# Kernel tuning notes

Measured on AMD Instinct MI355X. Metric: run time of the kernel, lower is better.

Reference implementation:

```python
import jax, jax.numpy as jnp
import numpy as np

D = 2048        # hidden_size
F = 1024        # moe_intermediate_size
E = 16          # num_experts
TOP_K = 2       # num_experts_per_tok
NORM_TOPK = True
B, S = 2, 1024


def setup_inputs() -> dict:
    key = jax.random.key(0)
    ks = jax.random.split(key, 6)
    scale = 0.02
    x = jax.random.normal(ks[0], (B, S, D), jnp.float32)
    w_gate = jax.random.normal(ks[1], (D, E), jnp.float32) * scale          # gate Linear (no bias)
    w_g = jax.random.normal(ks[2], (E, D, F), jnp.float32) * scale          # SwitchGLU gate_proj
    w_u = jax.random.normal(ks[3], (E, D, F), jnp.float32) * scale          # SwitchGLU up_proj
    w_d = jax.random.normal(ks[4], (E, F, D), jnp.float32) * scale          # SwitchGLU down_proj
    expert_bias = jnp.zeros((E,), jnp.float32)                              # nn.Parameter(zeros)
    return {"x": x, "w_gate": w_gate, "w_g": w_g, "w_u": w_u, "w_d": w_d,
            "expert_bias": expert_bias}


def reference(x, w_gate, w_g, w_u, w_d, expert_bias):
    xf = x.reshape(-1, D)  # [T, D] flatten tokens
    T = xf.shape[0]
    # routing: softmax in fp32, bias added AFTER softmax (as in source)
    gates = jax.nn.softmax((xf @ w_gate).astype(jnp.float32), axis=-1) + expert_bias
    scores, inds = jax.lax.top_k(gates, TOP_K)  # values gathered from biased gates
    if NORM_TOPK:
        scores = scores / (jnp.sum(scores, axis=-1, keepdims=True) + 1e-20)
    scores = scores.astype(x.dtype)
    # scatter top-k weights into dense [T, E] combine matrix (top-k inds are distinct)
    cw = jnp.zeros((T, E), x.dtype).at[jnp.arange(T)[:, None], inds].add(scores)
    # scan over experts: each step one gated-SiLU MLP + weighted accumulate
    def step(acc, inp):
        wg, wu, wd, w = inp  # wg/wu [D,F], wd [F,D], w [T]
        h = jax.nn.silu(xf @ wg) * (xf @ wu)  # [T, F]
        return acc + w[:, None] * (h @ wd), None
    y, _ = jax.lax.scan(step, jnp.zeros_like(xf), (w_g, w_u, w_d, cw.T))
    return y.reshape(x.shape)
```

## Files before the change

### kernel.cpp

```cpp
#include <hip/hip_runtime.h>
#include <hip/hip_bf16.h>

#define D_DIM 2048
#define F_DIM 1024
#define E_NUM 16
#define T_TOK 2048

typedef float f32x4 __attribute__((ext_vector_type(4)));
typedef short short8 __attribute__((ext_vector_type(8)));

__device__ inline unsigned pk2bf(float a, float b) {
    __hip_bfloat162 h2 = __float22bfloat162_rn(make_float2(a, b));
    union { __hip_bfloat162 h; unsigned u; } c; c.h = h2; return c.u;
}

__global__ __launch_bounds__(64) void k_route(const float* __restrict__ x,
                                              const float* __restrict__ wg,
                                              const float* __restrict__ bias,
                                              int* __restrict__ topk_idx,
                                              float* __restrict__ topk_w,
                                              int* __restrict__ counts) {
    int t = blockIdx.x;
    int l = threadIdx.x;
    int e = l & 15, c = l >> 4;
    const float* xr = x + (size_t)t * D_DIM + c * (D_DIM / 4);
    const float* wr = wg + (size_t)(c * (D_DIM / 4)) * E_NUM + e;
    float acc = 0.f;
#pragma unroll 4
    for (int d = 0; d < D_DIM / 4; ++d) acc += xr[d] * wr[(size_t)d * E_NUM];
    acc += __shfl_xor(acc, 16);
    acc += __shfl_xor(acc, 32);
    float m = acc;
#pragma unroll
    for (int s = 1; s < 16; s <<= 1) m = fmaxf(m, __shfl_xor(m, s));
    float p = __expf(acc - m);
    float sum = p;
#pragma unroll
    for (int s = 1; s < 16; s <<= 1) sum += __shfl_xor(sum, s);
    p = p / sum + bias[e];
    float v1 = p; int i1 = e;
#pragma unroll
    for (int s = 1; s < 16; s <<= 1) {
        float ov = __shfl_xor(v1, s); int oi = __shfl_xor(i1, s);
        if (ov > v1 || (ov == v1 && oi < i1)) { v1 = ov; i1 = oi; }
    }
    float v2 = (e == i1) ? -1e30f : p; int i2 = e;
#pragma unroll
    for (int s = 1; s < 16; s <<= 1) {
        float ov = __shfl_xor(v2, s); int oi = __shfl_xor(i2, s);
        if (ov > v2 || (ov == v2 && oi < i2)) { v2 = ov; i2 = oi; }
    }
    if (l == 0) {
        float s2 = v1 + v2 + 1e-20f;
        topk_idx[2 * t] = i1; topk_idx[2 * t + 1] = i2;
        topk_w[2 * t] = v1 / s2; topk_w[2 * t + 1] = v2 / s2;
        atomicAdd(&counts[i1], 1);
        atomicAdd(&counts[i2], 1);
    }
}

__global__ void k_offsets(const int* __restrict__ counts, int* __restrict__ offsets,
                          int* __restrict__ cursors) {
    if (threadIdx.x == 0) {
        int run = 0;
        for (int e = 0; e < E_NUM; ++e) { offsets[e] = run; cursors[e] = run; run += counts[e]; }
        offsets[E_NUM] = run;
    }
}

__global__ void k_scatter(const int* __restrict__ topk_idx, const float* __restrict__ topk_w,
                          int* __restrict__ cursors, int* __restrict__ token_ids,
                          float* __restrict__ slot_w) {
    int i = blockIdx.x * blockDim.x + threadIdx.x;
    if (i >= T_TOK * 2) return;
    int e = topk_idx[i];
    int slot = atomicAdd(&cursors[e], 1);
    token_ids[slot] = i >> 1;
    slot_w[slot] = topk_w[i];
}

__global__ __launch_bounds__(256, 4) void k_gateup(const float* __restrict__ x,
                                                   const float* __restrict__ wg_all,
                                                   const float* __restrict__ wu_all,
                                                   const int* __restrict__ offsets,
                                                   const int* __restrict__ token_ids,
                                                   __hip_bfloat16* __restrict__ hbuf) {
    int e = blockIdx.z;
    int off = offsets[e];
    int n_e = offsets[e + 1] - off;
    int m0 = blockIdx.y * 64;
    if (m0 >= n_e) return;
    int n0 = blockIdx.x * 64;
    const float* wg = wg_all + (size_t)e * (D_DIM * F_DIM);
    const float* wu = wu_all + (size_t)e * (D_DIM * F_DIM);

    __shared__ unsigned short As[2][64 * 40];
    __shared__ unsigned short Bs[2][2][64 * 40];

    int tid = threadIdx.x;
    int wid = tid >> 6, lane = tid & 63;
    int q = lane >> 4, nl = lane & 15;
    int wr = wid >> 1, wc = wid & 1;

    int arow = tid >> 2, acg = (tid & 3) * 8;
    int ag = m0 + arow;
    bool avalid = ag < n_e;
    const float* xrow = x + (size_t)token_ids[off + (avalid ? ag : 0)] * D_DIM;
    int bkr = (tid >> 4) * 2;
    int bcol = (tid & 15) * 4;

    f32x4 ra[2], rg[2], ru[2];
    f32x4 accG[2][2], accU[2][2];
#pragma unroll
    for (int ms = 0; ms < 2; ++ms)
#pragma unroll
        for (int ns = 0; ns < 2; ++ns) {
            accG[ms][ns] = (f32x4){0.f, 0.f, 0.f, 0.f};
            accU[ms][ns] = (f32x4){0.f, 0.f, 0.f, 0.f};
        }

    auto loadG = [&](int k0) {
        ra[0] = avalid ? *(const f32x4*)(xrow + k0 + acg) : (f32x4){0.f, 0.f, 0.f, 0.f};
        ra[1] = avalid ? *(const f32x4*)(xrow + k0 + acg + 4) : (f32x4){0.f, 0.f, 0.f, 0.f};
        size_t o0 = (size_t)(k0 + bkr) * F_DIM + n0 + bcol;
        rg[0] = *(const f32x4*)(wg + o0);
        rg[1] = *(const f32x4*)(wg + o0 + F_DIM);
        ru[0] = *(const f32x4*)(wu + o0);
        ru[1] = *(const f32x4*)(wu + o0 + F_DIM);
    };
    auto writeL = [&](int b) {
        union { short8 v; unsigned u[4]; } w0;
        w0.u[0] = pk2bf(ra[0].x, ra[0].y); w0.u[1] = pk2bf(ra[0].z, ra[0].w);
        w0.u[2] = pk2bf(ra[1].x, ra[1].y); w0.u[3] = pk2bf(ra[1].z, ra[1].w);
        *(short8*)&As[b][arow * 40 + acg] = w0.v;
#pragma unroll
        for (int j = 0; j < 4; ++j) {
            int col = bcol + j;
            int kk = bkr ^ (((col >> 3) & 3) << 3);
            *(unsigned*)&Bs[b][0][col * 40 + kk] = pk2bf(rg[0][j], rg[1][j]);
            *(unsigned*)&Bs[b][1][col * 40 + kk] = pk2bf(ru[0][j], ru[1][j]);
        }
    };
    auto compute = [&](int b) {
        short8 af[2];
#pragma unroll
        for (int ms = 0; ms < 2; ++ms)
            af[ms] = *(const short8*)&As[b][(wr * 32 + ms * 16 + nl) * 40 + q * 8];
#pragma unroll
        for (int ns = 0; ns < 2; ++ns) {
            int col = wc * 32 + ns * 16 + nl;
            int colb = col * 40 + 8 * (q ^ ((col >> 3) & 3));
            short8 bg = *(const short8*)&Bs[b][0][colb];
            short8 bu = *(const short8*)&Bs[b][1][colb];
#pragma unroll
            for (int ms = 0; ms < 2; ++ms) {
                accG[ms][ns] = __builtin_amdgcn_mfma_f32_16x16x32_bf16(af[ms], bg, accG[ms][ns], 0, 0, 0);
                accU[ms][ns] = __builtin_amdgcn_mfma_f32_16x16x32_bf16(af[ms], bu, accU[ms][ns], 0, 0, 0);
            }
        }
    };

    loadG(0);
    writeL(0);
    __syncthreads();
    for (int t = 0; t < D_DIM / 32; ++t) {
        int b = t & 1;
        if (t < D_DIM / 32 - 1) loadG((t + 1) * 32);
        compute(b);
        if (t < D_DIM / 32 - 1) writeL(b ^ 1);
        __syncthreads();
    }

#pragma unroll
    for (int ms = 0; ms < 2; ++ms)
#pragma unroll
        for (int j = 0; j < 4; ++j) {
            int g2 = m0 + wr * 32 + ms * 16 + q * 4 + j;
            if (g2 < n_e) {
                size_t hbase = (size_t)(off + g2) * F_DIM;
#pragma unroll
                for (int ns = 0; ns < 2; ++ns) {
                    float g = accG[ms][ns][j];
                    float u = accU[ms][ns][j];
                    float hv = (g / (1.f + __expf(-g))) * u;
                    hbuf[hbase + n0 + wc * 32 + ns * 16 + nl] = __float2bfloat16(hv);
                }
            }
        }
}

__global__ __launch_bounds__(256, 4) void k_down(const __hip_bfloat16* __restrict__ hbuf,
                                                 const float* __restrict__ wd_all,
                                                 const int* __restrict__ offsets,
                                                 const int* __restrict__ token_ids,
                                                 const float* __restrict__ slot_w,
                                                 float* __restrict__ y) {
    int e = blockIdx.z;
    int off = offsets[e];
    int n_e = offsets[e + 1] - off;
    int m0 = blockIdx.y * 64;
    if (m0 >= n_e) return;
    int n0 = blockIdx.x * 64;
    const float* wd = wd_all + (size_t)e * (F_DIM * D_DIM);

    __shared__ unsigned short As[2][64 * 40];
    __shared__ unsigned short Bs[2][64 * 40];

    int tid = threadIdx.x;
    int wid = tid >> 6, lane = tid & 63;
    int q = lane >> 4, nl = lane & 15;
    int wr = wid >> 1, wc = wid & 1;

    int arow = tid >> 2, acg = (tid & 3) * 8;
    int ag = m0 + arow;
    bool avalid = ag < n_e;
    const unsigned short* hrow = (const unsigned short*)hbuf + (size_t)(off + (avalid ? ag : 0)) * F_DIM;
    int bkr = (tid >> 4) * 2;
    int bcol = (tid & 15) * 4;

    short8 rh;
    f32x4 rd[2];
    f32x4 acc[2][2];
#pragma unroll
    for (int ms = 0; ms < 2; ++ms)
#pragma unroll
        for (int ns = 0; ns < 2; ++ns) acc[ms][ns] = (f32x4){0.f, 0.f, 0.f, 0.f};

    auto loadG = [&](int k0) {
        rh = avalid ? *(const short8*)(hrow + k0 + acg) : (short8){0, 0, 0, 0, 0, 0, 0, 0};
        size_t o0 = (size_t)(k0 + bkr) * D_DIM + n0 + bcol;
        rd[0] = *(const f32x4*)(wd + o0);
        rd[1] = *(const f32x4*)(wd + o0 + D_DIM);
    };
    auto writeL = [&](int b) {
        *(short8*)&As[b][arow * 40 + acg] = rh;
#pragma unroll
        for (int j = 0; j < 4; ++j) {
            int col = bcol + j;
            int kk = bkr ^ (((col >> 3) & 3) << 3);
            *(unsigned*)&Bs[b][col * 40 + kk] = pk2bf(rd[0][j], rd[1][j]);
        }
    };
    auto compute = [&](int b) {
        short8 af[2];
#pragma unroll
        for (int ms = 0; ms < 2; ++ms)
            af[ms] = *(const short8*)&As[b][(wr * 32 + ms * 16 + nl) * 40 + q * 8];
#pragma unroll
        for (int ns = 0; ns < 2; ++ns) {
            int col = wc * 32 + ns * 16 + nl;
            short8 bd = *(const short8*)&Bs[b][col * 40 + 8 * (q ^ ((col >> 3) & 3))];
#pragma unroll
            for (int ms = 0; ms < 2; ++ms)
                acc[ms][ns] = __builtin_amdgcn_mfma_f32_16x16x32_bf16(af[ms], bd, acc[ms][ns], 0, 0, 0);
        }
    };

    loadG(0);
    writeL(0);
    __syncthreads();
    for (int t = 0; t < F_DIM / 32; ++t) {
        int b = t & 1;
        if (t < F_DIM / 32 - 1) loadG((t + 1) * 32);
        compute(b);
        if (t < F_DIM / 32 - 1) writeL(b ^ 1);
        __syncthreads();
    }

#pragma unroll
    for (int ms = 0; ms < 2; ++ms)
#pragma unroll
        for (int j = 0; j < 4; ++j) {
            int g2 = m0 + wr * 32 + ms * 16 + q * 4 + j;
            if (g2 < n_e) {
                float w2 = slot_w[off + g2];
                int t = token_ids[off + g2];
#pragma unroll
                for (int ns = 0; ns < 2; ++ns)
                    atomicAdd(&y[(size_t)t * D_DIM + n0 + wc * 32 + ns * 16 + nl], acc[ms][ns][j] * w2);
            }
        }
}

extern "C" void kernel_launch(void* const* d_in, const int* in_sizes, int n_in,
                              void* d_out, int out_size, void* d_ws, size_t ws_size,
                              hipStream_t stream) {
    const float* x      = (const float*)d_in[0];
    const float* w_gate = (const float*)d_in[1];
    const float* w_g    = (const float*)d_in[2];
    const float* w_u    = (const float*)d_in[3];
    const float* w_d    = (const float*)d_in[4];
    const float* bias   = (const float*)d_in[5];
    float* y = (float*)d_out;

    char* ws = (char*)d_ws;
    int*   counts    = (int*)(ws + 0);
    int*   offsets   = (int*)(ws + 64);
    int*   cursors   = (int*)(ws + 192);
    int*   topk_idx  = (int*)(ws + 256);
    float* topk_w    = (float*)(ws + 256 + 16384);
    int*   token_ids = (int*)(ws + 256 + 32768);
    float* slot_w    = (float*)(ws + 256 + 49152);
    __hip_bfloat16* hbuf = (__hip_bfloat16*)(ws + 66048);

    hipMemsetAsync(ws, 0, 256, stream);
    hipMemsetAsync(d_out, 0, (size_t)out_size * sizeof(float), stream);

    k_route<<<T_TOK, 64, 0, stream>>>(x, w_gate, bias, topk_idx, topk_w, counts);
    k_offsets<<<1, 64, 0, stream>>>(counts, offsets, cursors);
    k_scatter<<<(T_TOK * 2 + 255) / 256, 256, 0, stream>>>(topk_idx, topk_w, cursors, token_ids, slot_w);
    k_gateup<<<dim3(F_DIM / 64, 32, E_NUM), 256, 0, stream>>>(x, w_g, w_u, offsets, token_ids, hbuf);
    k_down<<<dim3(D_DIM / 64, 32, E_NUM), 256, 0, stream>>>(hbuf, w_d, offsets, token_ids, slot_w, y);
}
```

Measured before the change: 372.4 us.

## Give each wave a private LDS weight tile and load activations straight to registers

Both expert GEMM kernels drop the block-shared, double-buffered LDS tiles and the per-iteration __syncthreads. Each wavefront now stages its own 32-column slice of the weight tile in a private LDS buffer and reads its activation rows (x or hbuf) directly from global memory into MFMA operand registers. This is meant to remove block-wide barrier stalls and A-tile LDS traffic. In exchange, weight tiles are fetched and converted twice per block and activations are re-read by two waves each. The activation loads are also not prefetched, so their latency sits right before the MFMAs. Launch bounds are lowered from 4 to 3 blocks per CU.

```diff
diff --git a/kernel.cpp b/kernel.cpp
--- a/kernel.cpp
+++ b/kernel.cpp
@@ -8,6 +8,7 @@
 
 typedef float f32x4 __attribute__((ext_vector_type(4)));
 typedef short short8 __attribute__((ext_vector_type(8)));
+typedef unsigned uint2v __attribute__((ext_vector_type(2)));
 
 __device__ inline unsigned pk2bf(float a, float b) {
     __hip_bfloat162 h2 = __float22bfloat162_rn(make_float2(a, b));
@@ -79,7 +80,7 @@
     slot_w[slot] = topk_w[i];
 }
 
-__global__ __launch_bounds__(256, 4) void k_gateup(const float* __restrict__ x,
+__global__ __launch_bounds__(256, 3) void k_gateup(const float* __restrict__ x,
                                                    const float* __restrict__ wg_all,
                                                    const float* __restrict__ wu_all,
                                                    const int* __restrict__ offsets,
@@ -94,22 +95,26 @@
     const float* wg = wg_all + (size_t)e * (D_DIM * F_DIM);
     const float* wu = wu_all + (size_t)e * (D_DIM * F_DIM);
 
-    __shared__ unsigned short As[2][64 * 40];
-    __shared__ unsigned short Bs[2][2][64 * 40];
+    __shared__ unsigned short Bs[4][2][32 * 40];
 
     int tid = threadIdx.x;
     int wid = tid >> 6, lane = tid & 63;
     int q = lane >> 4, nl = lane & 15;
     int wr = wid >> 1, wc = wid & 1;
-
-    int arow = tid >> 2, acg = (tid & 3) * 8;
-    int ag = m0 + arow;
-    bool avalid = ag < n_e;
-    const float* xrow = x + (size_t)token_ids[off + (avalid ? ag : 0)] * D_DIM;
-    int bkr = (tid >> 4) * 2;
-    int bcol = (tid & 15) * 4;
-
-    f32x4 ra[2], rg[2], ru[2];
+    int colbase = n0 + wc * 32;
+
+    int r0 = m0 + wr * 32 + nl;
+    int r1 = r0 + 16;
+    const float* xr0 = x + (size_t)token_ids[off + (r0 < n_e ? r0 : 0)] * D_DIM;
+    const float* xr1 = x + (size_t)token_ids[off + (r1 < n_e ? r1 : 0)] * D_DIM;
+
+    int cg = lane & 7;
+    int kb4 = (lane >> 3) * 4;
+    const float* pg0 = wg + (size_t)kb4 * F_DIM + colbase + cg * 4;
+    const float* pu0 = wu + (size_t)kb4 * F_DIM + colbase + cg * 4;
+    unsigned short* BG = &Bs[wid][0][0];
+    unsigned short* BU = &Bs[wid][1][0];
+
     f32x4 accG[2][2], accU[2][2];
 #pragma unroll
     for (int ms = 0; ms < 2; ++ms)
@@ -119,77 +124,77 @@
             accU[ms][ns] = (f32x4){0.f, 0.f, 0.f, 0.f};
         }
 
-    auto loadG = [&](int k0) {
-        ra[0] = avalid ? *(const f32x4*)(xrow + k0 + acg) : (f32x4){0.f, 0.f, 0.f, 0.f};
-        ra[1] = avalid ? *(const f32x4*)(xrow + k0 + acg + 4) : (f32x4){0.f, 0.f, 0.f, 0.f};
-        size_t o0 = (size_t)(k0 + bkr) * F_DIM + n0 + bcol;
-        rg[0] = *(const f32x4*)(wg + o0);
-        rg[1] = *(const f32x4*)(wg + o0 + F_DIM);
-        ru[0] = *(const f32x4*)(wu + o0);
-        ru[1] = *(const f32x4*)(wu + o0 + F_DIM);
-    };
-    auto writeL = [&](int b) {
-        union { short8 v; unsigned u[4]; } w0;
-        w0.u[0] = pk2bf(ra[0].x, ra[0].y); w0.u[1] = pk2bf(ra[0].z, ra[0].w);
-        w0.u[2] = pk2bf(ra[1].x, ra[1].y); w0.u[3] = pk2bf(ra[1].z, ra[1].w);
-        *(short8*)&As[b][arow * 40 + acg] = w0.v;
+    f32x4 g0, g1, g2, g3, u0, u1, u2, u3;
+    auto loadW = [&](int k0) {
+        const float* pg = pg0 + (size_t)k0 * F_DIM;
+        const float* pu = pu0 + (size_t)k0 * F_DIM;
+        g0 = *(const f32x4*)pg; g1 = *(const f32x4*)(pg + F_DIM);
+        g2 = *(const f32x4*)(pg + 2 * F_DIM); g3 = *(const f32x4*)(pg + 3 * F_DIM);
+        u0 = *(const f32x4*)pu; u1 = *(const f32x4*)(pu + F_DIM);
+        u2 = *(const f32x4*)(pu + 2 * F_DIM); u3 = *(const f32x4*)(pu + 3 * F_DIM);
+    };
+    auto writeW = [&]() {
 #pragma unroll
         for (int j = 0; j < 4; ++j) {
-            int col = bcol + j;
-            int kk = bkr ^ (((col >> 3) & 3) << 3);
-            *(unsigned*)&Bs[b][0][col * 40 + kk] = pk2bf(rg[0][j], rg[1][j]);
-            *(unsigned*)&Bs[b][1][col * 40 + kk] = pk2bf(ru[0][j], ru[1][j]);
-        }
-    };
-    auto compute = [&](int b) {
-        short8 af[2];
-#pragma unroll
-        for (int ms = 0; ms < 2; ++ms)
-            af[ms] = *(const short8*)&As[b][(wr * 32 + ms * 16 + nl) * 40 + q * 8];
+            int col = cg * 4 + j;
+            int kk = kb4 ^ (((col >> 3) & 3) << 3);
+            uint2v vg, vu;
+            vg[0] = pk2bf(g0[j], g1[j]); vg[1] = pk2bf(g2[j], g3[j]);
+            vu[0] = pk2bf(u0[j], u1[j]); vu[1] = pk2bf(u2[j], u3[j]);
+            *(uint2v*)&BG[col * 40 + kk] = vg;
+            *(uint2v*)&BU[col * 40 + kk] = vu;
+        }
+    };
+    auto compute = [&](int k0) {
+        f32x4 a00 = *(const f32x4*)(xr0 + k0 + q * 8);
+        f32x4 a01 = *(const f32x4*)(xr0 + k0 + q * 8 + 4);
+        f32x4 a10 = *(const f32x4*)(xr1 + k0 + q * 8);
+        f32x4 a11 = *(const f32x4*)(xr1 + k0 + q * 8 + 4);
+        union { short8 v; unsigned u[4]; } af0, af1;
+        af0.u[0] = pk2bf(a00.x, a00.y); af0.u[1] = pk2bf(a00.z, a00.w);
+        af0.u[2] = pk2bf(a01.x, a01.y); af0.u[3] = pk2bf(a01.z, a01.w);
+        af1.u[0] = pk2bf(a10.x, a10.y); af1.u[1] = pk2bf(a10.z, a10.w);
+        af1.u[2] = pk2bf(a11.x, a11.y); af1.u[3] = pk2bf(a11.z, a11.w);
 #pragma unroll
         for (int ns = 0; ns < 2; ++ns) {
-            int col = wc * 32 + ns * 16 + nl;
-            int colb = col * 40 + 8 * (q ^ ((col >> 3) & 3));
-            short8 bg = *(const short8*)&Bs[b][0][colb];
-            short8 bu = *(const short8*)&Bs[b][1][colb];
-#pragma unroll
-            for (int ms = 0; ms < 2; ++ms) {
-                accG[ms][ns] = __builtin_amdgcn_mfma_f32_16x16x32_bf16(af[ms], bg, accG[ms][ns], 0, 0, 0);
-                accU[ms][ns] = __builtin_amdgcn_mfma_f32_16x16x32_bf16(af[ms], bu, accU[ms][ns], 0, 0, 0);
-            }
-        }
-    };
-
-    loadG(0);
-    writeL(0);
-    __syncthreads();
+            int col = ns * 16 + nl;
+            int cb = col * 40 + 8 * (q ^ ((col >> 3) & 3));
+            short8 bg = *(const short8*)&BG[cb];
+            short8 bu = *(const short8*)&BU[cb];
+            accG[0][ns] = __builtin_amdgcn_mfma_f32_16x16x32_bf16(af0.v, bg, accG[0][ns], 0, 0, 0);
+            accG[1][ns] = __builtin_amdgcn_mfma_f32_16x16x32_bf16(af1.v, bg, accG[1][ns], 0, 0, 0);
+            accU[0][ns] = __builtin_amdgcn_mfma_f32_16x16x32_bf16(af0.v, bu, accU[0][ns], 0, 0, 0);
+            accU[1][ns] = __builtin_amdgcn_mfma_f32_16x16x32_bf16(af1.v, bu, accU[1][ns], 0, 0, 0);
+        }
+    };
+
+    loadW(0);
+    writeW();
     for (int t = 0; t < D_DIM / 32; ++t) {
-        int b = t & 1;
-        if (t < D_DIM / 32 - 1) loadG((t + 1) * 32);
-        compute(b);
-        if (t < D_DIM / 32 - 1) writeL(b ^ 1);
-        __syncthreads();
+        if (t < D_DIM / 32 - 1) loadW((t + 1) * 32);
+        compute(t * 32);
+        if (t < D_DIM / 32 - 1) writeW();
     }
 
 #pragma unroll
     for (int ms = 0; ms < 2; ++ms)
 #pragma unroll
         for (int j = 0; j < 4; ++j) {
-            int g2 = m0 + wr * 32 + ms * 16 + q * 4 + j;
-            if (g2 < n_e) {
-                size_t hbase = (size_t)(off + g2) * F_DIM;
+            int g2r = m0 + wr * 32 + ms * 16 + q * 4 + j;
+            if (g2r < n_e) {
+                size_t hbase = (size_t)(off + g2r) * F_DIM;
 #pragma unroll
                 for (int ns = 0; ns < 2; ++ns) {
                     float g = accG[ms][ns][j];
                     float u = accU[ms][ns][j];
                     float hv = (g / (1.f + __expf(-g))) * u;
-                    hbuf[hbase + n0 + wc * 32 + ns * 16 + nl] = __float2bfloat16(hv);
+                    hbuf[hbase + colbase + ns * 16 + nl] = __float2bfloat16(hv);
                 }
             }
         }
 }
 
-__global__ __launch_bounds__(256, 4) void k_down(const __hip_bfloat16* __restrict__ hbuf,
+__global__ __launch_bounds__(256, 3) void k_down(const __hip_bfloat16* __restrict__ hbuf,
                                                  const float* __restrict__ wd_all,
                                                  const int* __restrict__ offsets,
                                                  const int* __restrict__ token_ids,
@@ -203,81 +208,77 @@
     int n0 = blockIdx.x * 64;
     const float* wd = wd_all + (size_t)e * (F_DIM * D_DIM);
 
-    __shared__ unsigned short As[2][64 * 40];
-    __shared__ unsigned short Bs[2][64 * 40];
+    __shared__ unsigned short Bs[4][32 * 40];
 
     int tid = threadIdx.x;
     int wid = tid >> 6, lane = tid & 63;
     int q = lane >> 4, nl = lane & 15;
     int wr = wid >> 1, wc = wid & 1;
-
-    int arow = tid >> 2, acg = (tid & 3) * 8;
-    int ag = m0 + arow;
-    bool avalid = ag < n_e;
-    const unsigned short* hrow = (const unsigned short*)hbuf + (size_t)(off + (avalid ? ag : 0)) * F_DIM;
-    int bkr = (tid >> 4) * 2;
-    int bcol = (tid & 15) * 4;
-
-    short8 rh;
-    f32x4 rd[2];
+    int colbase = n0 + wc * 32;
+
+    int r0 = m0 + wr * 32 + nl;
+    int r1 = r0 + 16;
+    const unsigned short* h0 = (const unsigned short*)hbuf + (size_t)(off + (r0 < n_e ? r0 : 0)) * F_DIM;
+    const unsigned short* h1 = (const unsigned short*)hbuf + (size_t)(off + (r1 < n_e ? r1 : 0)) * F_DIM;
+
+    int cg = lane & 7;
+    int kb4 = (lane >> 3) * 4;
+    const float* pd0 = wd + (size_t)kb4 * D_DIM + colbase + cg * 4;
+    unsigned short* BD = &Bs[wid][0];
+
     f32x4 acc[2][2];
 #pragma unroll
     for (int ms = 0; ms < 2; ++ms)
 #pragma unroll
         for (int ns = 0; ns < 2; ++ns) acc[ms][ns] = (f32x4){0.f, 0.f, 0.f, 0.f};
 
-    auto loadG = [&](int k0) {
-        rh = avalid ? *(const short8*)(hrow + k0 + acg) : (short8){0, 0, 0, 0, 0, 0, 0, 0};
-        size_t o0 = (size_t)(k0 + bkr) * D_DIM + n0 + bcol;
-        rd[0] = *(const f32x4*)(wd + o0);
-        rd[1] = *(const f32x4*)(wd + o0 + D_DIM);
-    };
-    auto writeL = [&](int b) {
-        *(short8*)&As[b][arow * 40 + acg] = rh;
+    f32x4 d0, d1, d2, d3;
+    auto loadW = [&](int k0) {
+        const float* pd = pd0 + (size_t)k0 * D_DIM;
+        d0 = *(const f32x4*)pd; d1 = *(const f32x4*)(pd + D_DIM);
+        d2 = *(const f32x4*)(pd + 2 * D_DIM); d3 = *(const f32x4*)(pd + 3 * D_DIM);
+    };
+    auto writeW = [&]() {
 #pragma unroll
         for (int j = 0; j < 4; ++j) {
-            int col = bcol + j;
-            int kk = bkr ^ (((col >> 3) & 3) << 3);
-            *(unsigned*)&Bs[b][col * 40 + kk] = pk2bf(rd[0][j], rd[1][j]);
-        }
-    };
-    auto compute = [&](int b) {
-        short8 af[2];
-#pragma unroll
-        for (int ms = 0; ms < 2; ++ms)
-            af[ms] = *(const short8*)&As[b][(wr * 32 + ms * 16 + nl) * 40 + q * 8];
+            int col = cg * 4 + j;
+            int kk = kb4 ^ (((col >> 3) & 3) << 3);
+            uint2v vd;
+            vd[0] = pk2bf(d0[j], d1[j]); vd[1] = pk2bf(d2[j], d3[j]);
+            *(uint2v*)&BD[col * 40 + kk] = vd;
+        }
+    };
+    auto compute = [&](int k0) {
+        short8 af0 = *(const short8*)(h0 + k0 + q * 8);
+        short8 af1 = *(const short8*)(h1 + k0 + q * 8);
 #pragma unroll
         for (int ns = 0; ns < 2; ++ns) {
-            int col = wc * 32 + ns * 16 + nl;
-            short8 bd = *(const short8*)&Bs[b][col * 40 + 8 * (q ^ ((col >> 3) & 3))];
-#pragma unroll
-            for (int ms = 0; ms < 2; ++ms)
-                acc[ms][ns] = __builtin_amdgcn_mfma_f32_16x16x32_bf16(af[ms], bd, acc[ms][ns], 0, 0, 0);
-        }
-    };
-
-    loadG(0);
-    writeL(0);
-    __syncthreads();
+            int col = ns * 16 + nl;
+            short8 bd = *(const short8*)&BD[col * 40 + 8 * (q ^ ((col >> 3) & 3))];
+            acc[0][ns] = __builtin_amdgcn_mfma_f32_16x16x32_bf16(af0, bd, acc[0][ns], 0, 0, 0);
+            acc[1][ns] = __builtin_amdgcn_mfma_f32_16x16x32_bf16(af1, bd, acc[1][ns], 0, 0, 0);
+        }
+    };
+
+    loadW(0);
+    writeW();
     for (int t = 0; t < F_DIM / 32; ++t) {
-        int b = t & 1;
-        if (t < F_DIM / 32 - 1) loadG((t + 1) * 32);
-        compute(b);
-        if (t < F_DIM / 32 - 1) writeL(b ^ 1);
-        __syncthreads();
+        if (t < F_DIM / 32 - 1) loadW((t + 1) * 32);
+        compute(t * 32);
+        if (t < F_DIM / 32 - 1) writeW();
     }
 
 #pragma unroll
     for (int ms = 0; ms < 2; ++ms)
 #pragma unroll
         for (int j = 0; j < 4; ++j) {
-            int g2 = m0 + wr * 32 + ms * 16 + q * 4 + j;
-            if (g2 < n_e) {
-                float w2 = slot_w[off + g2];
-                int t = token_ids[off + g2];
+            int g2r = m0 + wr * 32 + ms * 16 + q * 4 + j;
+            if (g2r < n_e) {
+                float w2 = slot_w[off + g2r];
+                int t = token_ids[off + g2r];
 #pragma unroll
                 for (int ns = 0; ns < 2; ++ns)
-                    atomicAdd(&y[(size_t)t * D_DIM + n0 + wc * 32 + ns * 16 + nl], acc[ms][ns][j] * w2);
+                    atomicAdd(&y[(size_t)t * D_DIM + colbase + ns * 16 + nl], acc[ms][ns][j] * w2);
             }
         }
 }
```

New measurement: 558.7 us. +50.0%, slower.

## Pre-gather tokens to bf16 buffer and remap block order across XCDs

Applied to the files above, without the earlier changes.

Adds a gather kernel that copies each routed token's row into a contiguous bf16 buffer, so the gate/up GEMM reads packed bf16 rows directly and no longer does the per-row token_ids indirection or the fp32-to-bf16 conversion on the A operand. Both GEMMs now use a flattened 1D grid, and the block index is remapped with a stride of 8 so that blocks sharing the same expert and weight columns are likely placed on the same XCD and its L2. Out-of-range rows are clamped to the last valid slot instead of being zero-filled, so they read real data whose results must be masked out at the output. This costs one extra kernel launch and an 8MB bf16 intermediate.

```diff
diff --git a/kernel.cpp b/kernel.cpp
--- a/kernel.cpp
+++ b/kernel.cpp
@@ -5,6 +5,7 @@
 #define F_DIM 1024
 #define E_NUM 16
 #define T_TOK 2048
+#define NSLOT (T_TOK * 2)
 
 typedef float f32x4 __attribute__((ext_vector_type(4)));
 typedef short short8 __attribute__((ext_vector_type(8)));
@@ -72,25 +73,41 @@
                           int* __restrict__ cursors, int* __restrict__ token_ids,
                           float* __restrict__ slot_w) {
     int i = blockIdx.x * blockDim.x + threadIdx.x;
-    if (i >= T_TOK * 2) return;
+    if (i >= NSLOT) return;
     int e = topk_idx[i];
     int slot = atomicAdd(&cursors[e], 1);
     token_ids[slot] = i >> 1;
     slot_w[slot] = topk_w[i];
 }
 
-__global__ __launch_bounds__(256, 4) void k_gateup(const float* __restrict__ x,
+__global__ __launch_bounds__(256) void k_gather(const float* __restrict__ x,
+                                                const int* __restrict__ token_ids,
+                                                __hip_bfloat16* __restrict__ xg) {
+    int s = blockIdx.x;
+    const float* src = x + (size_t)token_ids[s] * D_DIM + threadIdx.x * 8;
+    f32x4 a = *(const f32x4*)src;
+    f32x4 b = *(const f32x4*)(src + 4);
+    union { short8 v; unsigned u[4]; } w;
+    w.u[0] = pk2bf(a.x, a.y); w.u[1] = pk2bf(a.z, a.w);
+    w.u[2] = pk2bf(b.x, b.y); w.u[3] = pk2bf(b.z, b.w);
+    *(short8*)((unsigned short*)xg + (size_t)s * D_DIM + threadIdx.x * 8) = w.v;
+}
+
+__global__ __launch_bounds__(256, 4) void k_gateup(const __hip_bfloat16* __restrict__ xg,
                                                    const float* __restrict__ wg_all,
                                                    const float* __restrict__ wu_all,
                                                    const int* __restrict__ offsets,
-                                                   const int* __restrict__ token_ids,
                                                    __hip_bfloat16* __restrict__ hbuf) {
-    int e = blockIdx.z;
+    unsigned b0 = blockIdx.x;
+    unsigned w = (b0 & 7) * 1024u + (b0 >> 3);
+    int mi = w & 31;
+    int ni = (w >> 5) & 15;
+    int e  = w >> 9;
     int off = offsets[e];
     int n_e = offsets[e + 1] - off;
-    int m0 = blockIdx.y * 64;
+    int m0 = mi * 64;
     if (m0 >= n_e) return;
-    int n0 = blockIdx.x * 64;
+    int n0 = ni * 64;
     const float* wg = wg_all + (size_t)e * (D_DIM * F_DIM);
     const float* wu = wu_all + (size_t)e * (D_DIM * F_DIM);
 
@@ -103,13 +120,13 @@
     int wr = wid >> 1, wc = wid & 1;
 
     int arow = tid >> 2, acg = (tid & 3) * 8;
-    int ag = m0 + arow;
-    bool avalid = ag < n_e;
-    const float* xrow = x + (size_t)token_ids[off + (avalid ? ag : 0)] * D_DIM;
+    int sg = off + m0 + arow; if (sg > NSLOT - 1) sg = NSLOT - 1;
+    const unsigned short* xrow = (const unsigned short*)xg + (size_t)sg * D_DIM;
     int bkr = (tid >> 4) * 2;
     int bcol = (tid & 15) * 4;
 
-    f32x4 ra[2], rg[2], ru[2];
+    short8 rA;
+    f32x4 rg[2], ru[2];
     f32x4 accG[2][2], accU[2][2];
 #pragma unroll
     for (int ms = 0; ms < 2; ++ms)
@@ -120,8 +137,7 @@
         }
 
     auto loadG = [&](int k0) {
-        ra[0] = avalid ? *(const f32x4*)(xrow + k0 + acg) : (f32x4){0.f, 0.f, 0.f, 0.f};
-        ra[1] = avalid ? *(const f32x4*)(xrow + k0 + acg + 4) : (f32x4){0.f, 0.f, 0.f, 0.f};
+        rA = *(const short8*)(xrow + k0 + acg);
         size_t o0 = (size_t)(k0 + bkr) * F_DIM + n0 + bcol;
         rg[0] = *(const f32x4*)(wg + o0);
         rg[1] = *(const f32x4*)(wg + o0 + F_DIM);
@@ -129,10 +145,7 @@
         ru[1] = *(const f32x4*)(wu + o0 + F_DIM);
     };
     auto writeL = [&](int b) {
-        union { short8 v; unsigned u[4]; } w0;
-        w0.u[0] = pk2bf(ra[0].x, ra[0].y); w0.u[1] = pk2bf(ra[0].z, ra[0].w);
-        w0.u[2] = pk2bf(ra[1].x, ra[1].y); w0.u[3] = pk2bf(ra[1].z, ra[1].w);
-        *(short8*)&As[b][arow * 40 + acg] = w0.v;
+        *(short8*)&As[b][arow * 40 + acg] = rA;
 #pragma unroll
         for (int j = 0; j < 4; ++j) {
             int col = bcol + j;
@@ -195,12 +208,16 @@
                                                  const int* __restrict__ token_ids,
                                                  const float* __restrict__ slot_w,
                                                  float* __restrict__ y) {
-    int e = blockIdx.z;
+    unsigned b0 = blockIdx.x;
+    unsigned w = (b0 & 7) * 2048u + (b0 >> 3);
+    int mi = w & 31;
+    int ni = (w >> 5) & 31;
+    int e  = w >> 10;
     int off = offsets[e];
     int n_e = offsets[e + 1] - off;
-    int m0 = blockIdx.y * 64;
+    int m0 = mi * 64;
     if (m0 >= n_e) return;
-    int n0 = blockIdx.x * 64;
+    int n0 = ni * 64;
     const float* wd = wd_all + (size_t)e * (F_DIM * D_DIM);
 
     __shared__ unsigned short As[2][64 * 40];
@@ -212,9 +229,8 @@
     int wr = wid >> 1, wc = wid & 1;
 
     int arow = tid >> 2, acg = (tid & 3) * 8;
-    int ag = m0 + arow;
-    bool avalid = ag < n_e;
-    const unsigned short* hrow = (const unsigned short*)hbuf + (size_t)(off + (avalid ? ag : 0)) * F_DIM;
+    int sg = off + m0 + arow; if (sg > NSLOT - 1) sg = NSLOT - 1;
+    const unsigned short* hrow = (const unsigned short*)hbuf + (size_t)sg * F_DIM;
     int bkr = (tid >> 4) * 2;
     int bcol = (tid & 15) * 4;
 
@@ -227,7 +243,7 @@
         for (int ns = 0; ns < 2; ++ns) acc[ms][ns] = (f32x4){0.f, 0.f, 0.f, 0.f};
 
     auto loadG = [&](int k0) {
-        rh = avalid ? *(const short8*)(hrow + k0 + acg) : (short8){0, 0, 0, 0, 0, 0, 0, 0};
+        rh = *(const short8*)(hrow + k0 + acg);
         size_t o0 = (size_t)(k0 + bkr) * D_DIM + n0 + bcol;
         rd[0] = *(const f32x4*)(wd + o0);
         rd[1] = *(const f32x4*)(wd + o0 + D_DIM);
@@ -302,13 +318,15 @@
     int*   token_ids = (int*)(ws + 256 + 32768);
     float* slot_w    = (float*)(ws + 256 + 49152);
     __hip_bfloat16* hbuf = (__hip_bfloat16*)(ws + 66048);
+    __hip_bfloat16* xg   = (__hip_bfloat16*)(ws + 66048 + 8388608);
 
     hipMemsetAsync(ws, 0, 256, stream);
     hipMemsetAsync(d_out, 0, (size_t)out_size * sizeof(float), stream);
 
     k_route<<<T_TOK, 64, 0, stream>>>(x, w_gate, bias, topk_idx, topk_w, counts);
     k_offsets<<<1, 64, 0, stream>>>(counts, offsets, cursors);
-    k_scatter<<<(T_TOK * 2 + 255) / 256, 256, 0, stream>>>(topk_idx, topk_w, cursors, token_ids, slot_w);
-    k_gateup<<<dim3(F_DIM / 64, 32, E_NUM), 256, 0, stream>>>(x, w_g, w_u, offsets, token_ids, hbuf);
-    k_down<<<dim3(D_DIM / 64, 32, E_NUM), 256, 0, stream>>>(hbuf, w_d, offsets, token_ids, slot_w, y);
-}
+    k_scatter<<<(NSLOT + 255) / 256, 256, 0, stream>>>(topk_idx, topk_w, cursors, token_ids, slot_w);
+    k_gather<<<NSLOT, 256, 0, stream>>>(x, token_ids, xg);
+    k_gateup<<<16 * 32 * E_NUM, 256, 0, stream>>>(xg, w_g, w_u, offsets, hbuf);
+    k_down<<<32 * 32 * E_NUM, 256, 0, stream>>>(hbuf, w_d, offsets, token_ids, slot_w, y);
+}
```

Measured after the change: 375.2 us. Within noise of the previous version (+0.8%).
